# Optimization experiments

Hardware: AMD Instinct MI355X
Metric: run time of the kernel (lower is better)

## Reference

```python
import jax, jax.numpy as jnp
import numpy as np
import math

N, FB, D, H, HD, L, K = 512, 256, 64, 128, 4, 4, 100
# note: H=num_heads=4, HD=head_dim=128 -> inner dim H*HD = 512
H, HD = 4, 128
HHD = H * HD
EPS = 1e-5


def mish(x):
    return x * jnp.tanh(jax.nn.softplus(x))


def layer_norm(x, g, b):
    mu = jnp.mean(x, axis=-1, keepdims=True)
    var = jnp.var(x, axis=-1, keepdims=True)
    return (x - mu) * jax.lax.rsqrt(var + EPS) * g + b


def setup_inputs() -> dict:
    key = jax.random.key(0)
    ks = jax.random.split(key, 16)
    def lin(k, fan_in, shape):
        return jax.random.normal(k, shape, jnp.float32) / np.sqrt(fan_in)
    return {
        "node_features": jax.random.normal(ks[0], (N, FB), jnp.float32),
        "amds": jax.random.uniform(ks[1], (N, K), jnp.float32),
        "emb_W": lin(ks[2], FB, (FB, D)),
        "emb_b": jnp.zeros((D,), jnp.float32),
        "bias_emb_W": lin(ks[3], K, (K, D)),
        "bias_emb_b": jnp.zeros((D,), jnp.float32),
        "ln1_g": jnp.ones((D,), jnp.float32),
        "ln1_b": jnp.zeros((D,), jnp.float32),
        "ln2_g": jnp.ones((D,), jnp.float32),
        "ln2_b": jnp.zeros((D,), jnp.float32),
        "qkv_W": lin(ks[4], D, (L, D, 3 * HHD)),
        "qkv_b": jnp.zeros((L, 3 * HHD), jnp.float32),
        "diff_W": lin(ks[5], D, (L, D, HHD)),
        "diff_b": jnp.zeros((L, HHD), jnp.float32),
        "o_W": lin(ks[6], HHD, (L, HHD, D)),
        "o_b": jnp.zeros((L, D), jnp.float32),
        "bout_W": lin(ks[7], HHD, (L, HHD, D)),
        "bout_b": jnp.zeros((L, D), jnp.float32),
        "out_W": lin(ks[8], D, (D, 1)),
        "out_b": jnp.zeros((1,), jnp.float32),
    }


def reference(node_features, amds, emb_W, emb_b, bias_emb_W, bias_emb_b,
              ln1_g, ln1_b, ln2_g, ln2_b, qkv_W, qkv_b, diff_W, diff_b,
              o_W, o_b, bout_W, bout_b, out_W, out_b):
    h = node_features @ emb_W + emb_b                     # [N, D]
    b0 = amds @ bias_emb_W + bias_emb_b                   # [N, D]
    bias = b0[None, :, :] - b0[:, None, :]                # [N, N, D]
    x = layer_norm(h, ln1_g, ln1_b)
    scale = 1.0 / math.sqrt(HD)
    for l in range(L):
        qkv = (x @ qkv_W[l] + qkv_b[l]).reshape(N, H, 3 * HD)
        q, k, v = jnp.split(qkv, 3, axis=-1)              # each [N, H, HD]
        be = mish(bias @ diff_W[l] + diff_b[l])           # [N, N, H*HD]
        diffs = jnp.linalg.norm(be.reshape(N, N, H, HD), axis=-1)  # [N, N, H]
        diffs = jnp.transpose(diffs, (2, 0, 1))           # [H, N, N]
        logits = jnp.einsum('nhd,mhd->hnm', q, k) * scale + diffs
        attn = jax.nn.softmax(logits, axis=-1)            # [H, N, N]
        vals = jnp.einsum('hnm,mhd->nhd', attn, v).reshape(N, HHD)
        temp_x = vals @ o_W[l] + o_b[l]                   # [N, D]
        bias = mish(be @ bout_W[l] + bout_b[l])           # [N, N, D]
        x = layer_norm(x + temp_x, ln2_g, ln2_b)
    return x @ out_W + out_b                              # [N, 1]
```

## Files before the change

kernel.cpp:

```cpp
#include <hip/hip_runtime.h>
#include <hip/hip_bf16.h>
#include <hip/hip_fp16.h>
#include <cmath>


namespace {

constexpr int kN   = 512;
constexpr int kD   = 64;
constexpr int kH   = 4;
constexpr int kHD  = 128;
constexpr int kHHD = 512;
constexpr int kFB  = 256;
constexpr int kK   = 100;
constexpr float kEps   = 1e-5f;
constexpr float kScale = 0.08838834764831845f;

typedef unsigned short u16;
typedef unsigned int u32;
typedef short bf16x8 __attribute__((ext_vector_type(8)));
typedef _Float16 f16x8 __attribute__((ext_vector_type(8)));
typedef float f32x4 __attribute__((ext_vector_type(4)));

__device__ __forceinline__ float mish_f(float x) {
    float e  = __expf(x);
    float n2 = fmaf(e, e + 2.0f, 2.0f);
    return fmaf(x + x, -__builtin_amdgcn_rcpf(n2), x);
}

__device__ __forceinline__ u32 pkh(float a, float b) {
    union { __half2 h; u32 u; } cv;
    cv.h = __float22half2_rn(make_float2(a, b));
    return cv.u;
}
__device__ __forceinline__ f16x8 mkh8(u32 a, u32 b, u32 c, u32 d) {
    union { u32 w[4]; f16x8 v; } cv;
    cv.w[0] = a; cv.w[1] = b; cv.w[2] = c; cv.w[3] = d;
    return cv.v;
}
__device__ __forceinline__ u16 f16_bits(float f) {
    union { __half h; u16 u; } cv;
    cv.h = __float2half(f);
    return cv.u;
}

__global__ __launch_bounds__(64) void embed_kernel(
    const float* __restrict__ nf, const float* __restrict__ amds,
    const float* __restrict__ emb_W, const float* __restrict__ emb_b,
    const float* __restrict__ bemb_W, const float* __restrict__ bemb_b,
    const float* __restrict__ ln1_g, const float* __restrict__ ln1_b,
    float* __restrict__ x, float* __restrict__ b0)
{
    const int n = blockIdx.x;
    const int d = threadIdx.x;
    __shared__ float s_row[kFB];
    #pragma unroll
    for (int r = 0; r < kFB / kD; ++r) s_row[r * kD + d] = nf[n * kFB + r * kD + d];
    __syncthreads();
    float acc = emb_b[d];
    for (int k = 0; k < kFB; ++k) acc = fmaf(s_row[k], emb_W[k * kD + d], acc);
    float mu = acc;
    #pragma unroll
    for (int off = 32; off > 0; off >>= 1) mu += __shfl_xor(mu, off);
    mu *= (1.0f / kD);
    float dv = acc - mu;
    float var = dv * dv;
    #pragma unroll
    for (int off = 32; off > 0; off >>= 1) var += __shfl_xor(var, off);
    var *= (1.0f / kD);
    x[n * kD + d] = dv * rsqrtf(var + kEps) * ln1_g[d] + ln1_b[d];
    __syncthreads();
    s_row[d] = amds[n * kK + d];
    if (d < kK - kD) s_row[kD + d] = amds[n * kK + kD + d];
    __syncthreads();
    float bacc = bemb_b[d];
    for (int k = 0; k < kK; ++k) bacc = fmaf(s_row[k], bemb_W[k * kD + d], bacc);
    b0[n * kD + d] = bacc;
}

__global__ __launch_bounds__(256) void bias_init_kernel(
    const float* __restrict__ b0, u16* __restrict__ bias)
{
    int gid = blockIdx.x * 256 + threadIdx.x;
    int d8 = gid & 7;
    int j  = (gid >> 3) & (kN - 1);
    int i  = gid >> 12;
    const float4* bj = (const float4*)(b0 + j * kD + d8 * 8);
    const float4* bi = (const float4*)(b0 + i * kD + d8 * 8);
    float4 a0 = bj[0], a1 = bj[1];
    float4 c0 = bi[0], c1 = bi[1];
    union { u32 w[4]; bf16x8 v; } cv;
    cv.w[0] = pkh(a0.x - c0.x, a0.y - c0.y);
    cv.w[1] = pkh(a0.z - c0.z, a0.w - c0.w);
    cv.w[2] = pkh(a1.x - c1.x, a1.y - c1.y);
    cv.w[3] = pkh(a1.z - c1.z, a1.w - c1.w);
    *(bf16x8*)(bias + (long)gid * 8) = cv.v;
}

__global__ __launch_bounds__(256) void prep_weights_kernel(
    const float* __restrict__ diff_W, const float* __restrict__ bout_W,
    u16* __restrict__ dWt, u16* __restrict__ boutWt)
{
    int gid = blockIdx.x * 256 + threadIdx.x;
    if (gid < 4 * 32768) {
        int e = gid;
        int l = e >> 15;
        int r = e & 32767;
        int k = r >> 9;
        int n = r & 511;
        dWt[l * 32768 + n * 64 + k] = f16_bits(diff_W[e]);
    } else {
        int e = gid - 4 * 32768;
        int l = e >> 15;
        int r = e & 32767;
        int k = r >> 6;
        int d = r & 63;
        boutWt[l * 32768 + d * 512 + k] = f16_bits(bout_W[e]);
    }
}

__global__ __launch_bounds__(256) void qkv_kernel(
    const float* __restrict__ x, const float* __restrict__ W,
    const float* __restrict__ b, float* __restrict__ qkv)
{
    const int t  = threadIdx.x;
    const int c  = blockIdx.x * 256 + t;
    const int n0 = blockIdx.y * 8;
    __shared__ float s_x[8 * kD];
    s_x[t]       = x[n0 * kD + t];
    s_x[256 + t] = x[n0 * kD + 256 + t];
    __syncthreads();
    float acc[8];
    float bb = b[c];
    #pragma unroll
    for (int r = 0; r < 8; ++r) acc[r] = bb;
    for (int d = 0; d < kD; ++d) {
        float wv = W[d * (3 * kHHD) + c];
        #pragma unroll
        for (int r = 0; r < 8; ++r) acc[r] = fmaf(s_x[r * kD + d], wv, acc[r]);
    }
    #pragma unroll
    for (int r = 0; r < 8; ++r) qkv[(n0 + r) * (3 * kHHD) + c] = acc[r];
}

__global__ __launch_bounds__(256, 2) void bias_layer_mfma(
    u16* __restrict__ bias,
    const u16* __restrict__ dWt, const u16* __restrict__ boutWt,
    const float* __restrict__ diff_b, const float* __restrict__ bout_b,
    float* __restrict__ diffs, int last)
{
    __shared__ u16 s_w[2][4096];
    __shared__ float s_db[kHHD];

    const int t    = threadIdx.x;
    const int w    = t >> 6;
    const int lane = t & 63;
    const int q    = lane >> 4;
    const int c    = lane & 15;
    const int pb   = blockIdx.x * 128 + w * 32;

    const int sb_bc  = t >> 3;
    const int sb_kb  = t & 7;
    const int sr     = ((sb_bc >> 2) & 1) * 16 + ((sb_bc >> 3) << 2) + (sb_bc & 3);
    const int w1_dst = sr * 64 + (sb_kb ^ (sr & 7)) * 8;
    const int sb_d   = t >> 2;
    const int sb_k2  = t & 3;
    const int w2_dst = 2048 + sb_d * 32 + (sb_k2 ^ ((sb_d >> 1) & 3)) * 8;
    const u16* g_w1 = dWt + sb_bc * 64 + sb_kb * 8;
    const u16* g_w2 = boutWt + sb_d * 512 + sb_k2 * 8;

    f16x8 Bf[2][2];
    #pragma unroll
    for (int mt = 0; mt < 2; ++mt) {
        #pragma unroll
        for (int s = 0; s < 2; ++s) {
            Bf[mt][s] = *(const f16x8*)(bias + (long)(pb + mt * 16 + c) * kD + s * 32 + q * 8);
        }
    }

    {
        bf16x8 r0 = *(const bf16x8*)g_w1;
        bf16x8 r1 = *(const bf16x8*)g_w2;
        *(bf16x8*)&s_w[0][w1_dst] = r0;
        *(bf16x8*)&s_w[0][w2_dst] = r1;
        s_db[t] = diff_b[t];
        s_db[256 + t] = diff_b[256 + t];
    }
    __syncthreads();

    f32x4 acc2[2][4];
    #pragma unroll
    for (int mt = 0; mt < 2; ++mt)
        #pragma unroll
        for (int dg = 0; dg < 4; ++dg) acc2[mt][dg] = (f32x4)0.0f;
    float psum[2][4];
    #pragma unroll
    for (int mt = 0; mt < 2; ++mt)
        #pragma unroll
        for (int h = 0; h < 4; ++h) psum[mt][h] = 0.0f;

    const int sw1 = c & 7;
    const int sw2 = (c >> 1) & 3;
    int cur = 0;

    for (int g2 = 0; g2 < 16; ++g2) {
        bf16x8 r0, r1;
        if (g2 < 15) {
            r0 = *(const bf16x8*)(g_w1 + (g2 + 1) * 2048);
            r1 = *(const bf16x8*)(g_w2 + (g2 + 1) * 32);
        }

        f32x4 a1[2][2];
        #pragma unroll
        for (int mt = 0; mt < 2; ++mt)
            #pragma unroll
            for (int u = 0; u < 2; ++u) a1[mt][u] = (f32x4)0.0f;
        const u16* w1 = &s_w[cur][0];
        #pragma unroll
        for (int u = 0; u < 2; ++u) {
            int row = (u * 16 + c) * 64;
            int o0 = row + ((0 + q) ^ sw1) * 8;
            int o1 = row + ((4 + q) ^ sw1) * 8;
            f16x8 A0 = *(const f16x8*)(w1 + o0);
            f16x8 A1 = *(const f16x8*)(w1 + o1);
            #pragma unroll
            for (int mt = 0; mt < 2; ++mt) {
                a1[mt][u] = __builtin_amdgcn_mfma_f32_16x16x32_f16(A0, Bf[mt][0], a1[mt][u], 0, 0, 0);
                a1[mt][u] = __builtin_amdgcn_mfma_f32_16x16x32_f16(A1, Bf[mt][1], a1[mt][u], 0, 0, 0);
            }
        }

        const int hd = g2 >> 2;
        const float4 db0 = *(const float4*)&s_db[g2 * 32 + q * 8];
        const float4 db1 = *(const float4*)&s_db[g2 * 32 + q * 8 + 4];
        f16x8 A2[2];
        #pragma unroll
        for (int mt = 0; mt < 2; ++mt) {
            u32 p[2][2];
            #pragma unroll
            for (int u = 0; u < 2; ++u) {
                const float4 db = u ? db1 : db0;
                float v0 = mish_f(a1[mt][u][0] + db.x);
                float v1 = mish_f(a1[mt][u][1] + db.y);
                float v2 = mish_f(a1[mt][u][2] + db.z);
                float v3 = mish_f(a1[mt][u][3] + db.w);
                psum[mt][hd] += v0 * v0 + v1 * v1 + v2 * v2 + v3 * v3;
                p[u][0] = pkh(v0, v1);
                p[u][1] = pkh(v2, v3);
            }
            A2[mt] = mkh8(p[0][0], p[0][1], p[1][0], p[1][1]);
        }

        if (!last) {
            const u16* w2 = &s_w[cur][2048];
            const int kb2 = (q ^ sw2) * 8;
            #pragma unroll
            for (int dg = 0; dg < 4; ++dg) {
                int bo = dg * 512 + c * 32 + kb2;
                f16x8 Wf = *(const f16x8*)(w2 + bo);
                #pragma unroll
                for (int mt = 0; mt < 2; ++mt) {
                    acc2[mt][dg] = __builtin_amdgcn_mfma_f32_16x16x32_f16(A2[mt], Wf, acc2[mt][dg], 0, 0, 0);
                }
            }
        }

        if (g2 < 15) {
            int nb = cur ^ 1;
            *(bf16x8*)&s_w[nb][w1_dst] = r0;
            *(bf16x8*)&s_w[nb][w2_dst] = r1;
            __syncthreads();
            cur = nb;
        }
    }

    if (!last) {
        #pragma unroll
        for (int mt = 0; mt < 2; ++mt) {
            #pragma unroll
            for (int dg = 0; dg < 4; ++dg) {
                float bb = bout_b[dg * 16 + c];
                #pragma unroll
                for (int r = 0; r < 4; ++r) {
                    float v = mish_f(acc2[mt][dg][r] + bb);
                    bias[(long)(pb + mt * 16 + 4 * q + r) * kD + dg * 16 + c] = f16_bits(v);
                }
            }
        }
    }
    const int i  = blockIdx.x >> 2;
    const int jb = (blockIdx.x & 3) * 128 + w * 32;
    #pragma unroll
    for (int mt = 0; mt < 2; ++mt) {
        #pragma unroll
        for (int h = 0; h < 4; ++h) {
            psum[mt][h] += __shfl_xor(psum[mt][h], 16);
            psum[mt][h] += __shfl_xor(psum[mt][h], 32);
        }
        float sv = (q == 0) ? psum[mt][0] : (q == 1) ? psum[mt][1]
                 : (q == 2) ? psum[mt][2] : psum[mt][3];
        diffs[q * (kN * kN) + i * kN + jb + mt * 16 + c] = sqrtf(sv);
    }
}

__global__ __launch_bounds__(256) void flash_attn_kernel(
    const float* __restrict__ qkv, const float* __restrict__ diffs,
    float* __restrict__ part, float* __restrict__ ml)
{
    __shared__ float s_a[16 * 132];
    __shared__ float s_b[128 * 36];

    const int t  = threadIdx.x;
    const int tx = t & 15;
    const int ty = t >> 4;
    const int n0 = blockIdx.x * 16;
    const int mq = blockIdx.y;
    const int h  = blockIdx.z;
    const int m0 = mq * 128;

    #pragma unroll
    for (int rep = 0; rep < 2; ++rep) {
        int f = rep * 256 + t;
        int row = f >> 5;
        int c4  = f & 31;
        *(float4*)&s_a[row * 132 + c4 * 4] =
            *(const float4*)&qkv[(n0 + row) * (3 * kHHD) + h * 384 + c4 * 4];
    }

    float acc[8];
    #pragma unroll
    for (int cc = 0; cc < 8; ++cc) acc[cc] = 0.0f;

    for (int db = 0; db < 4; ++db) {
        __syncthreads();
        #pragma unroll
        for (int rep = 0; rep < 4; ++rep) {
            int f = rep * 256 + t;
            int row = f >> 3;
            int c4  = f & 7;
            *(float4*)&s_b[row * 36 + c4 * 4] =
                *(const float4*)&qkv[(m0 + row) * (3 * kHHD) + h * 384 + 128 + db * 32 + c4 * 4];
        }
        __syncthreads();
        #pragma unroll 2
        for (int k4 = 0; k4 < 8; ++k4) {
            float4 a = *(const float4*)&s_a[ty * 132 + db * 32 + k4 * 4];
            #pragma unroll
            for (int cc = 0; cc < 8; ++cc) {
                float4 b = *(const float4*)&s_b[(tx + 16 * cc) * 36 + k4 * 4];
                acc[cc] = fmaf(a.x, b.x, acc[cc]);
                acc[cc] = fmaf(a.y, b.y, acc[cc]);
                acc[cc] = fmaf(a.z, b.z, acc[cc]);
                acc[cc] = fmaf(a.w, b.w, acc[cc]);
            }
        }
    }

    #pragma unroll
    for (int cc = 0; cc < 8; ++cc) {
        acc[cc] = acc[cc] * kScale +
                  diffs[h * (kN * kN) + (n0 + ty) * kN + m0 + tx + 16 * cc];
    }
    float mrow = acc[0];
    #pragma unroll
    for (int cc = 1; cc < 8; ++cc) mrow = fmaxf(mrow, acc[cc]);
    #pragma unroll
    for (int off = 1; off < 16; off <<= 1) mrow = fmaxf(mrow, __shfl_xor(mrow, off));
    float lrow = 0.0f;
    #pragma unroll
    for (int cc = 0; cc < 8; ++cc) {
        float p = __expf(acc[cc] - mrow);
        acc[cc] = p;
        lrow += p;
    }
    #pragma unroll
    for (int off = 1; off < 16; off <<= 1) lrow += __shfl_xor(lrow, off);

    __syncthreads();
    #pragma unroll
    for (int cc = 0; cc < 8; ++cc) s_a[ty * 132 + tx + 16 * cc] = acc[cc];
    if (tx == 0) {
        *(float2*)&ml[((h * 4 + mq) * kN + n0 + ty) * 2] = make_float2(mrow, lrow);
    }

    const int pbase = (h * 4 + mq) * (kN * kHD) + (n0 + ty) * kHD;
    for (int db = 0; db < 4; ++db) {
        __syncthreads();
        #pragma unroll
        for (int rep = 0; rep < 4; ++rep) {
            int f = rep * 256 + t;
            int row = f >> 3;
            int c4  = f & 7;
            *(float4*)&s_b[row * 36 + c4 * 4] =
                *(const float4*)&qkv[(m0 + row) * (3 * kHHD) + h * 384 + 256 + db * 32 + c4 * 4];
        }
        __syncthreads();
        float a0 = 0.0f, a1 = 0.0f;
        for (int c4 = 0; c4 < 32; ++c4) {
            float4 pa = *(const float4*)&s_a[ty * 132 + c4 * 4];
            #pragma unroll
            for (int u = 0; u < 4; ++u) {
                float pu = (u == 0) ? pa.x : (u == 1) ? pa.y : (u == 2) ? pa.z : pa.w;
                float2 vv = *(const float2*)&s_b[(c4 * 4 + u) * 36 + tx * 2];
                a0 = fmaf(pu, vv.x, a0);
                a1 = fmaf(pu, vv.y, a1);
            }
        }
        *(float2*)&part[pbase + db * 32 + tx * 2] = make_float2(a0, a1);
    }
}

__global__ __launch_bounds__(256) void oproj_ln_kernel(
    const float* __restrict__ part, const float* __restrict__ ml,
    const float* __restrict__ o_W, const float* __restrict__ o_b,
    const float* __restrict__ g2, const float* __restrict__ b2,
    float* __restrict__ x)
{
    const int n = blockIdx.x;
    const int t = threadIdx.x;
    const int w = t >> 6;
    const int d = t & 63;
    __shared__ float s_v[kHHD];
    __shared__ float s_part[4][kD];
    #pragma unroll
    for (int r = 0; r < 2; ++r) {
        int j  = r * 256 + t;
        int h  = j >> 7;
        int dd = j & 127;
        float2 m_l[4];
        float M = -1e30f;
        #pragma unroll
        for (int q = 0; q < 4; ++q) {
            m_l[q] = *(const float2*)&ml[((h * 4 + q) * kN + n) * 2];
            M = fmaxf(M, m_l[q].x);
        }
        float L = 0.0f, wq[4];
        #pragma unroll
        for (int q = 0; q < 4; ++q) {
            wq[q] = __expf(m_l[q].x - M);
            L = fmaf(wq[q], m_l[q].y, L);
        }
        float sv = 0.0f;
        #pragma unroll
        for (int q = 0; q < 4; ++q) {
            sv = fmaf(wq[q], part[(h * 4 + q) * (kN * kHD) + n * kHD + dd], sv);
        }
        s_v[j] = sv / L;
    }
    __syncthreads();
    float acc = 0.0f;
    #pragma unroll 4
    for (int j = 0; j < 128; ++j)
        acc = fmaf(s_v[w * 128 + j], o_W[(w * 128 + j) * kD + d], acc);
    s_part[w][d] = acc;
    __syncthreads();
    if (t < kD) {
        float av = o_b[d] + ((s_part[0][d] + s_part[1][d]) + (s_part[2][d] + s_part[3][d]));
        float xv = x[n * kD + d] + av;
        float mu = xv;
        #pragma unroll
        for (int off = 32; off > 0; off >>= 1) mu += __shfl_xor(mu, off);
        mu *= (1.0f / kD);
        float dv = xv - mu;
        float var = dv * dv;
        #pragma unroll
        for (int off = 32; off > 0; off >>= 1) var += __shfl_xor(var, off);
        var *= (1.0f / kD);
        x[n * kD + d] = dv * rsqrtf(var + kEps) * g2[d] + b2[d];
    }
}

__global__ __launch_bounds__(64) void final_kernel(
    const float* __restrict__ x, const float* __restrict__ out_W,
    const float* __restrict__ out_b, float* __restrict__ out)
{
    const int n = blockIdx.x * 64 + threadIdx.x;
    float acc = out_b[0];
    #pragma unroll
    for (int d = 0; d < kD; ++d) acc = fmaf(x[n * kD + d], out_W[d], acc);
    out[n] = acc;
}

}

extern "C" void kernel_launch(void* const* d_in, const int* in_sizes, int n_in,
                              void* d_out, int out_size, void* d_ws, size_t ws_size,
                              hipStream_t stream)
{
    (void)in_sizes; (void)n_in; (void)out_size; (void)ws_size;

    const float* nf     = (const float*)d_in[0];
    const float* amds   = (const float*)d_in[1];
    const float* emb_W  = (const float*)d_in[2];
    const float* emb_b  = (const float*)d_in[3];
    const float* bemb_W = (const float*)d_in[4];
    const float* bemb_b = (const float*)d_in[5];
    const float* ln1_g  = (const float*)d_in[6];
    const float* ln1_b  = (const float*)d_in[7];
    const float* ln2_g  = (const float*)d_in[8];
    const float* ln2_b  = (const float*)d_in[9];
    const float* qkv_W  = (const float*)d_in[10];
    const float* qkv_b  = (const float*)d_in[11];
    const float* diff_W = (const float*)d_in[12];
    const float* diff_b = (const float*)d_in[13];
    const float* o_W    = (const float*)d_in[14];
    const float* o_b    = (const float*)d_in[15];
    const float* bout_W = (const float*)d_in[16];
    const float* bout_b = (const float*)d_in[17];
    const float* out_W  = (const float*)d_in[18];
    const float* out_b  = (const float*)d_in[19];

    float* ws = (float*)d_ws;
    float* ws_x      = ws;
    float* ws_b0     = ws_x + 32768;
    float* ws_qkv    = ws_b0 + 32768;
    float* ws_ml     = ws_qkv + 786432;
    float* ws_diffs  = ws_ml + 262144;
    float* ws_part   = ws_diffs + 1048576;
    u16*   ws_bias   = (u16*)(ws_part + 1048576);
    u16*   dWt       = ws_bias + 16777216;
    u16*   boutWt    = dWt + 131072;

    embed_kernel<<<kN, kD, 0, stream>>>(nf, amds, emb_W, emb_b, bemb_W, bemb_b,
                                        ln1_g, ln1_b, ws_x, ws_b0);
    bias_init_kernel<<<(kN * kN * kD / 8) / 256, 256, 0, stream>>>(ws_b0, ws_bias);
    prep_weights_kernel<<<(2 * 4 * 32768) / 256, 256, 0, stream>>>(
        diff_W, bout_W, dWt, boutWt);

    for (int l = 0; l < 4; ++l) {
        qkv_kernel<<<dim3(6, 64), 256, 0, stream>>>(
            ws_x, qkv_W + l * kD * (3 * kHHD), qkv_b + l * (3 * kHHD), ws_qkv);
        bias_layer_mfma<<<kN * kN / 128, 256, 0, stream>>>(
            ws_bias, dWt + l * 32768, boutWt + l * 32768,
            diff_b + l * kHHD, bout_b + l * kD, ws_diffs, (l == 3) ? 1 : 0);
        flash_attn_kernel<<<dim3(32, 4, kH), 256, 0, stream>>>(
            ws_qkv, ws_diffs, ws_part, ws_ml);
        oproj_ln_kernel<<<kN, 256, 0, stream>>>(
            ws_part, ws_ml, o_W + l * kHHD * kD, o_b + l * kD, ln2_g, ln2_b, ws_x);
    }
    final_kernel<<<kN / kD, kD, 0, stream>>>(ws_x, out_W, out_b, (float*)d_out);
}
```

Before: 550.9 us.

## Register-block flash attention kernel with 4x4 per-thread tiles over 32 query rows

Each thread in the attention kernel now computes a 4-row by 4-column block of logits and a 4-row by 4-wide slice of the output. Each block covers 32 query rows instead of 16, and V is staged in full head-dim slabs of 32 keys. The aim is to cut LDS loads per FMA through register reuse and to widen output stores. In exchange the grid is halved to 256 blocks, which lowers parallelism, and register pressure goes up.

```diff
diff --git a/kernel.cpp b/kernel.cpp
--- a/kernel.cpp
+++ b/kernel.cpp
@@ -42,6 +42,21 @@
     union { __half h; u16 u; } cv;
     cv.h = __float2half(f);
     return cv.u;
+}
+
+__device__ __forceinline__ float dot4(float4 a, float4 b, float acc) {
+    acc = fmaf(a.x, b.x, acc);
+    acc = fmaf(a.y, b.y, acc);
+    acc = fmaf(a.z, b.z, acc);
+    acc = fmaf(a.w, b.w, acc);
+    return acc;
+}
+__device__ __forceinline__ float4 fma4(float s, float4 v, float4 d) {
+    d.x = fmaf(s, v.x, d.x);
+    d.y = fmaf(s, v.y, d.y);
+    d.z = fmaf(s, v.z, d.z);
+    d.w = fmaf(s, v.w, d.w);
+    return d;
 }
 
 __global__ __launch_bounds__(64) void embed_kernel(
@@ -307,19 +322,20 @@
     const float* __restrict__ qkv, const float* __restrict__ diffs,
     float* __restrict__ part, float* __restrict__ ml)
 {
-    __shared__ float s_a[16 * 132];
+    __shared__ float s_a[32 * 132];
     __shared__ float s_b[128 * 36];
 
     const int t  = threadIdx.x;
-    const int tx = t & 15;
-    const int ty = t >> 4;
-    const int n0 = blockIdx.x * 16;
+    const int tx = t & 31;
+    const int ty = t >> 5;
+    const int r0 = ty * 4;
+    const int n0 = blockIdx.x * 32;
     const int mq = blockIdx.y;
     const int h  = blockIdx.z;
     const int m0 = mq * 128;
 
     #pragma unroll
-    for (int rep = 0; rep < 2; ++rep) {
+    for (int rep = 0; rep < 4; ++rep) {
         int f = rep * 256 + t;
         int row = f >> 5;
         int c4  = f & 31;
@@ -327,87 +343,110 @@
             *(const float4*)&qkv[(n0 + row) * (3 * kHHD) + h * 384 + c4 * 4];
     }
 
-    float acc[8];
-    #pragma unroll
-    for (int cc = 0; cc < 8; ++cc) acc[cc] = 0.0f;
+    float acc[4][4];
+    #pragma unroll
+    for (int i = 0; i < 4; ++i)
+        #pragma unroll
+        for (int cc = 0; cc < 4; ++cc) acc[i][cc] = 0.0f;
 
     for (int db = 0; db < 4; ++db) {
         __syncthreads();
         #pragma unroll
         for (int rep = 0; rep < 4; ++rep) {
             int f = rep * 256 + t;
-            int row = f >> 3;
+            int col = f >> 3;
             int c4  = f & 7;
-            *(float4*)&s_b[row * 36 + c4 * 4] =
-                *(const float4*)&qkv[(m0 + row) * (3 * kHHD) + h * 384 + 128 + db * 32 + c4 * 4];
+            *(float4*)&s_b[col * 36 + c4 * 4] =
+                *(const float4*)&qkv[(m0 + col) * (3 * kHHD) + h * 384 + 128 + db * 32 + c4 * 4];
         }
         __syncthreads();
-        #pragma unroll 2
+        #pragma unroll
         for (int k4 = 0; k4 < 8; ++k4) {
-            float4 a = *(const float4*)&s_a[ty * 132 + db * 32 + k4 * 4];
-            #pragma unroll
-            for (int cc = 0; cc < 8; ++cc) {
-                float4 b = *(const float4*)&s_b[(tx + 16 * cc) * 36 + k4 * 4];
-                acc[cc] = fmaf(a.x, b.x, acc[cc]);
-                acc[cc] = fmaf(a.y, b.y, acc[cc]);
-                acc[cc] = fmaf(a.z, b.z, acc[cc]);
-                acc[cc] = fmaf(a.w, b.w, acc[cc]);
+            float4 a0 = *(const float4*)&s_a[(r0 + 0) * 132 + db * 32 + k4 * 4];
+            float4 a1 = *(const float4*)&s_a[(r0 + 1) * 132 + db * 32 + k4 * 4];
+            float4 a2 = *(const float4*)&s_a[(r0 + 2) * 132 + db * 32 + k4 * 4];
+            float4 a3 = *(const float4*)&s_a[(r0 + 3) * 132 + db * 32 + k4 * 4];
+            #pragma unroll
+            for (int cc = 0; cc < 4; ++cc) {
+                float4 b = *(const float4*)&s_b[(tx + 32 * cc) * 36 + k4 * 4];
+                acc[0][cc] = dot4(a0, b, acc[0][cc]);
+                acc[1][cc] = dot4(a1, b, acc[1][cc]);
+                acc[2][cc] = dot4(a2, b, acc[2][cc]);
+                acc[3][cc] = dot4(a3, b, acc[3][cc]);
             }
         }
     }
 
-    #pragma unroll
-    for (int cc = 0; cc < 8; ++cc) {
-        acc[cc] = acc[cc] * kScale +
-                  diffs[h * (kN * kN) + (n0 + ty) * kN + m0 + tx + 16 * cc];
-    }
-    float mrow = acc[0];
-    #pragma unroll
-    for (int cc = 1; cc < 8; ++cc) mrow = fmaxf(mrow, acc[cc]);
-    #pragma unroll
-    for (int off = 1; off < 16; off <<= 1) mrow = fmaxf(mrow, __shfl_xor(mrow, off));
-    float lrow = 0.0f;
-    #pragma unroll
-    for (int cc = 0; cc < 8; ++cc) {
-        float p = __expf(acc[cc] - mrow);
-        acc[cc] = p;
-        lrow += p;
-    }
-    #pragma unroll
-    for (int off = 1; off < 16; off <<= 1) lrow += __shfl_xor(lrow, off);
-
-    __syncthreads();
-    #pragma unroll
-    for (int cc = 0; cc < 8; ++cc) s_a[ty * 132 + tx + 16 * cc] = acc[cc];
-    if (tx == 0) {
-        *(float2*)&ml[((h * 4 + mq) * kN + n0 + ty) * 2] = make_float2(mrow, lrow);
-    }
-
-    const int pbase = (h * 4 + mq) * (kN * kHD) + (n0 + ty) * kHD;
-    for (int db = 0; db < 4; ++db) {
-        __syncthreads();
+    float mr[4], lr[4];
+    #pragma unroll
+    for (int i = 0; i < 4; ++i) {
+        const float* dro = diffs + h * (kN * kN) + (n0 + r0 + i) * kN + m0 + tx;
+        #pragma unroll
+        for (int cc = 0; cc < 4; ++cc)
+            acc[i][cc] = fmaf(acc[i][cc], kScale, dro[32 * cc]);
+        float m = fmaxf(fmaxf(acc[i][0], acc[i][1]), fmaxf(acc[i][2], acc[i][3]));
+        #pragma unroll
+        for (int off = 1; off < 32; off <<= 1) m = fmaxf(m, __shfl_xor(m, off));
+        mr[i] = m;
+        float l = 0.0f;
+        #pragma unroll
+        for (int cc = 0; cc < 4; ++cc) {
+            float p = __expf(acc[i][cc] - m);
+            acc[i][cc] = p;
+            l += p;
+        }
+        #pragma unroll
+        for (int off = 1; off < 32; off <<= 1) l += __shfl_xor(l, off);
+        lr[i] = l;
+    }
+
+    __syncthreads();
+    #pragma unroll
+    for (int i = 0; i < 4; ++i) {
+        #pragma unroll
+        for (int cc = 0; cc < 4; ++cc)
+            s_a[(r0 + i) * 132 + tx + 32 * cc] = acc[i][cc];
+        if (tx == 0)
+            *(float2*)&ml[((h * 4 + mq) * kN + n0 + r0 + i) * 2] = make_float2(mr[i], lr[i]);
+    }
+
+    float4 o0 = {0,0,0,0}, o1 = {0,0,0,0}, o2 = {0,0,0,0}, o3 = {0,0,0,0};
+    for (int ms = 0; ms < 4; ++ms) {
+        if (ms > 0) __syncthreads();
         #pragma unroll
         for (int rep = 0; rep < 4; ++rep) {
             int f = rep * 256 + t;
-            int row = f >> 3;
-            int c4  = f & 7;
-            *(float4*)&s_b[row * 36 + c4 * 4] =
-                *(const float4*)&qkv[(m0 + row) * (3 * kHHD) + h * 384 + 256 + db * 32 + c4 * 4];
+            int row = f >> 5;
+            int c4  = f & 31;
+            *(float4*)&s_b[row * 132 + c4 * 4] =
+                *(const float4*)&qkv[(m0 + ms * 32 + row) * (3 * kHHD) + h * 384 + 256 + c4 * 4];
         }
         __syncthreads();
-        float a0 = 0.0f, a1 = 0.0f;
-        for (int c4 = 0; c4 < 32; ++c4) {
-            float4 pa = *(const float4*)&s_a[ty * 132 + c4 * 4];
+        #pragma unroll
+        for (int k4 = 0; k4 < 8; ++k4) {
+            float4 p0 = *(const float4*)&s_a[(r0 + 0) * 132 + ms * 32 + k4 * 4];
+            float4 p1 = *(const float4*)&s_a[(r0 + 1) * 132 + ms * 32 + k4 * 4];
+            float4 p2 = *(const float4*)&s_a[(r0 + 2) * 132 + ms * 32 + k4 * 4];
+            float4 p3 = *(const float4*)&s_a[(r0 + 3) * 132 + ms * 32 + k4 * 4];
             #pragma unroll
             for (int u = 0; u < 4; ++u) {
-                float pu = (u == 0) ? pa.x : (u == 1) ? pa.y : (u == 2) ? pa.z : pa.w;
-                float2 vv = *(const float2*)&s_b[(c4 * 4 + u) * 36 + tx * 2];
-                a0 = fmaf(pu, vv.x, a0);
-                a1 = fmaf(pu, vv.y, a1);
+                float4 v = *(const float4*)&s_b[(k4 * 4 + u) * 132 + tx * 4];
+                float pu0 = (u == 0) ? p0.x : (u == 1) ? p0.y : (u == 2) ? p0.z : p0.w;
+                float pu1 = (u == 0) ? p1.x : (u == 1) ? p1.y : (u == 2) ? p1.z : p1.w;
+                float pu2 = (u == 0) ? p2.x : (u == 1) ? p2.y : (u == 2) ? p2.z : p2.w;
+                float pu3 = (u == 0) ? p3.x : (u == 1) ? p3.y : (u == 2) ? p3.z : p3.w;
+                o0 = fma4(pu0, v, o0);
+                o1 = fma4(pu1, v, o1);
+                o2 = fma4(pu2, v, o2);
+                o3 = fma4(pu3, v, o3);
             }
         }
-        *(float2*)&part[pbase + db * 32 + tx * 2] = make_float2(a0, a1);
-    }
+    }
+    const int pbase = (h * 4 + mq) * (kN * kHD) + (n0 + r0) * kHD + 4 * tx;
+    *(float4*)&part[pbase]            = o0;
+    *(float4*)&part[pbase + kHD]      = o1;
+    *(float4*)&part[pbase + 2 * kHD]  = o2;
+    *(float4*)&part[pbase + 3 * kHD]  = o3;
 }
 
 __global__ __launch_bounds__(256) void oproj_ln_kernel(
@@ -533,7 +572,7 @@
         bias_layer_mfma<<<kN * kN / 128, 256, 0, stream>>>(
             ws_bias, dWt + l * 32768, boutWt + l * 32768,
             diff_b + l * kHHD, bout_b + l * kD, ws_diffs, (l == 3) ? 1 : 0);
-        flash_attn_kernel<<<dim3(32, 4, kH), 256, 0, stream>>>(
+        flash_attn_kernel<<<dim3(16, 4, kH), 256, 0, stream>>>(
             ws_qkv, ws_diffs, ws_part, ws_ml);
         oproj_ln_kernel<<<kN, 256, 0, stream>>>(
             ws_part, ws_ml, o_W + l * kHHD * kD, o_b + l * kD, ln2_g, ln2_b, ws_x);
```

Measured after the change: 526.2 us. 4.5% less time.
